# Performance work log

Measured on AMD Instinct MI355X. Metric: run time of the kernel, lower is better.

## Reference

```python
import jax, jax.numpy as jnp
import numpy as np
from jax import lax

IMG_SIZE = 512        # efficientdet-d0 input resolution
TOP_K = 256           # fixed candidate count for jit-compatible NMS
THRESHOLD = 0.01      # score threshold (init kwarg)
IOU_THRESHOLD = 0.5   # NMS IoU threshold (init kwarg)


def make_anchors():
    """Standard EfficientDet-d0 anchors: P3-P7, 3 scales x 3 ratios, xyxy."""
    strides = [8, 16, 32, 64, 128]
    scales = [2.0 ** 0, 2.0 ** (1.0 / 3.0), 2.0 ** (2.0 / 3.0)]
    ratios = [0.5, 1.0, 2.0]
    base = 4.0
    out = []
    for s in strides:
        fs = IMG_SIZE // s
        xs = (np.arange(fs, dtype=np.float32) + 0.5) * s
        cy, cx = np.meshgrid(xs, xs, indexing='ij')
        for r in ratios:
            for sc in scales:
                w = base * s * sc * np.sqrt(1.0 / r)
                h = base * s * sc * np.sqrt(r)
                a = np.stack([cx - w / 2, cy - h / 2, cx + w / 2, cy + h / 2], -1)
                out.append(a.reshape(-1, 4))
    return np.concatenate(out, 0).astype(np.float32)  # [49104, 4]


def decode_boxes(anchors, regs):
    """RetinaNet-style delta decode. anchors [A,4] xyxy, regs [B,A,4]."""
    aw = anchors[:, 2] - anchors[:, 0]
    ah = anchors[:, 3] - anchors[:, 1]
    acx = anchors[:, 0] + 0.5 * aw
    acy = anchors[:, 1] + 0.5 * ah
    dx, dy, dw, dh = regs[..., 0], regs[..., 1], regs[..., 2], regs[..., 3]
    cx = acx + dx * aw
    cy = acy + dy * ah
    w = aw * jnp.exp(jnp.clip(dw, -4.0, 4.0))
    h = ah * jnp.exp(jnp.clip(dh, -4.0, 4.0))
    boxes = jnp.stack([cx - 0.5 * w, cy - 0.5 * h, cx + 0.5 * w, cy + 0.5 * h], -1)
    return jnp.clip(boxes, 0.0, float(IMG_SIZE))  # [B,A,4]


def pairwise_iou(boxes):
    """boxes [K,4] xyxy -> iou [K,K]."""
    area = jnp.maximum(boxes[:, 2] - boxes[:, 0], 0) * jnp.maximum(boxes[:, 3] - boxes[:, 1], 0)
    lt = jnp.maximum(boxes[:, None, :2], boxes[None, :, :2])
    rb = jnp.minimum(boxes[:, None, 2:], boxes[None, :, 2:])
    wh = jnp.maximum(rb - lt, 0.0)
    inter = wh[..., 0] * wh[..., 1]
    union = area[:, None] + area[None, :] - inter
    return inter / jnp.maximum(union, 1e-8)


def nms_keep(boxes, scores):
    """Sequential NMS over score-sorted candidates. boxes [K,4], scores [K]."""
    K = boxes.shape[0]
    iou = pairwise_iou(boxes)  # [K,K]
    ar = jnp.arange(K)
    keep0 = scores > 0.0

    def body(i, keep):
        suppressed = jnp.any(keep & (iou[:, i] > IOU_THRESHOLD) & (ar < i))
        return keep.at[i].set(keep[i] & ~suppressed)

    return lax.fori_loop(0, K, body, keep0)


def setup_inputs() -> dict:
    key = jax.random.key(0)
    k1, k2 = jax.random.split(key)
    B, A, C = 8, 49104, 80
    cls_logits = jax.random.normal(k1, (B, A, C), dtype=jnp.float32) - 2.0
    box_regs = 0.2 * jax.random.normal(k2, (B, A, 4), dtype=jnp.float32)
    anchors = jnp.asarray(make_anchors())
    return {"cls_logits": cls_logits, "box_regs": box_regs, "anchors": anchors}


def reference(cls_logits, box_regs, anchors):
    probs = jax.nn.sigmoid(cls_logits)            # [B,A,C]
    scores = probs.max(-1)                        # [B,A]
    labels = probs.argmax(-1)                     # [B,A]
    boxes = decode_boxes(anchors, box_regs)       # [B,A,4]
    scores = jnp.where(scores > THRESHOLD, scores, 0.0)
    top_s, idx = lax.top_k(scores, TOP_K)         # [B,K]
    top_b = jnp.take_along_axis(boxes, idx[..., None], axis=1)   # [B,K,4]
    top_l = jnp.take_along_axis(labels, idx, axis=1)             # [B,K]
    keep = jax.vmap(nms_keep)(top_b, top_s)                      # [B,K] bool
    keep_f = keep.astype(top_b.dtype)
    dets = jnp.concatenate([top_b * keep_f[..., None], (top_s * keep_f)[..., None]], -1)  # [B,K,5]
    return dets, top_l, keep
```

## Files before the change

### kernel.cpp

```cpp
#include <hip/hip_runtime.h>
#include <stdint.h>
#include <math.h>

#define IMGF   512.0f
#define A_N    49104
#define B_N    8
#define C_N    80
#define K_N    256
#define IOU_T  0.5f
#define NBIN   4096
#define CAP    2048

__device__ __forceinline__ int bin_of(uint32_t key) {
    float s = __uint_as_float(key);
    int b = (int)(s * 4096.0f);
    return b > 4095 ? 4095 : b;
}

__global__ __launch_bounds__(256) void score_kernel(
    const float* __restrict__ logits,
    uint32_t* __restrict__ keys)
{
    const int tid  = threadIdx.x;
    const int lane = tid & 63;
    const int grp  = lane >> 2, j = lane & 3;
    const int g = blockIdx.x * 64 + (tid >> 6) * 16 + grp;

    const float4* p = (const float4*)(logits + (size_t)g * C_N);
    float4 v0 = p[j], v1 = p[j + 4], v2 = p[j + 8], v3 = p[j + 12], v4 = p[j + 16];
    float m = fmaxf(fmaxf(fmaxf(v0.x, v0.y), fmaxf(v0.z, v0.w)),
                    fmaxf(fmaxf(v1.x, v1.y), fmaxf(v1.z, v1.w)));
    m = fmaxf(m, fmaxf(fmaxf(v2.x, v2.y), fmaxf(v2.z, v2.w)));
    m = fmaxf(m, fmaxf(fmaxf(v3.x, v3.y), fmaxf(v3.z, v3.w)));
    m = fmaxf(m, fmaxf(fmaxf(v4.x, v4.y), fmaxf(v4.z, v4.w)));
    m = fmaxf(m, __shfl_xor(m, 1, 64));
    m = fmaxf(m, __shfl_xor(m, 2, 64));
    if (j == 0) {
        float s = 1.0f / (1.0f + expf(-m));
        if (!(s > 0.01f)) s = 0.0f;
        keys[g] = __float_as_uint(s);
    }
}

__global__ __launch_bounds__(1024) void select_nms_kernel(
    const uint32_t* __restrict__ keys,
    const float* __restrict__ logits,
    const float* __restrict__ regs,
    const float* __restrict__ anchors,
    float* __restrict__ out)
{
    const int b   = blockIdx.x;
    const int tid = threadIdx.x;
    const int lane = tid & 63, wv = tid >> 6;

    __shared__ uint32_t hist[NBIN];
    __shared__ int wtots[16];
    __shared__ int sh_T, sh_nc;
    __shared__ unsigned long long cand[CAP];
    __shared__ unsigned long long sorted[K_N];
    __shared__ float4 sbox[K_N];
    __shared__ float  sscore[K_N];
    __shared__ int    slab[K_N];
    __shared__ unsigned long long supr[K_N][4];
    __shared__ unsigned long long keepw[4];

    const uint32_t* kb = keys + (size_t)b * A_N;
    const uint4* kb4 = (const uint4*)kb;
    const int N4 = A_N / 4;

    for (int i = tid; i < NBIN; i += 1024) hist[i] = 0;
    if (tid == 0) sh_nc = 0;
    __syncthreads();
    for (int i = tid; i < N4; i += 1024) {
        uint4 v = kb4[i];
        atomicAdd(&hist[bin_of(v.x)], 1u);
        atomicAdd(&hist[bin_of(v.y)], 1u);
        atomicAdd(&hist[bin_of(v.z)], 1u);
        atomicAdd(&hist[bin_of(v.w)], 1u);
    }
    __syncthreads();

    const int lo = tid * 4;
    int seg = (int)hist[lo] + (int)hist[lo + 1]
            + (int)hist[lo + 2] + (int)hist[lo + 3];
    int s1 = seg;
#pragma unroll
    for (int off = 1; off < 64; off <<= 1) {
        int v = __shfl_down(s1, off, 64);
        if (lane + off < 64) s1 += v;
    }
    if (lane == 0) wtots[wv] = s1;
    __syncthreads();
    int wsuf = 0;
    for (int w = wv + 1; w < 16; ++w) wsuf += wtots[w];
    int above = wsuf + (s1 - seg);
    if (above < K_N && above + seg >= K_N) {
        int cum = above;
        for (int bin = lo + 3; bin >= lo; --bin) {
            int c = (int)hist[bin];
            if (cum + c >= K_N) { sh_T = bin; break; }
            cum += c;
        }
    }
    __syncthreads();
    const int T = sh_T;

    for (int i = tid; i < N4; i += 1024) {
        uint4 v = kb4[i];
        uint32_t ks[4] = { v.x, v.y, v.z, v.w };
#pragma unroll
        for (int q = 0; q < 4; ++q) {
            if (bin_of(ks[q]) >= T) {
                int p = atomicAdd(&sh_nc, 1);
                if (p < CAP)
                    cand[p] = ((unsigned long long)ks[q] << 32)
                            | (unsigned long long)(0xFFFFFFFFu - (uint32_t)(4 * i + q));
            }
        }
    }
    if (tid < K_N) sorted[tid] = 0ull;
    __syncthreads();
    int nc = sh_nc; if (nc > CAP) nc = CAP;

    for (int i = tid; i < nc; i += 1024) {
        unsigned long long me = cand[i];
        int r = 0;
        for (int jq = 0; jq < nc; ++jq) r += (cand[jq] > me);
        if (r < K_N) sorted[r] = me;
    }
    __syncthreads();

    if (tid < K_N) {
#pragma clang fp contract(off)
        unsigned long long cv = sorted[tid];
        uint32_t key = (uint32_t)(cv >> 32);
        uint32_t ai  = 0xFFFFFFFFu - (uint32_t)cv;
        if (ai >= (uint32_t)A_N) ai = 0;
        int a = (int)ai;
        float s = __uint_as_float(key);
        sscore[tid] = s;

        {
            const float4* lp = (const float4*)(logits + ((size_t)b * A_N + a) * C_N);
            float best = -INFINITY; int cls = 0;
#pragma unroll
            for (int k = 0; k < 20; ++k) {
                float4 w = lp[k];
                if (w.x > best) { best = w.x; cls = 4 * k + 0; }
                if (w.y > best) { best = w.y; cls = 4 * k + 1; }
                if (w.z > best) { best = w.z; cls = 4 * k + 2; }
                if (w.w > best) { best = w.w; cls = 4 * k + 3; }
            }
            slab[tid] = cls;
        }

        float ax0 = anchors[4 * a + 0], ay0 = anchors[4 * a + 1];
        float ax1 = anchors[4 * a + 2], ay1 = anchors[4 * a + 3];
        float aw = ax1 - ax0, ah = ay1 - ay0;
        float acx = ax0 + 0.5f * aw, acy = ay0 + 0.5f * ah;
        const float* r = regs + ((size_t)b * A_N + a) * 4;
        float dx = r[0], dy = r[1], dw = r[2], dh = r[3];
        float cx = acx + dx * aw;
        float cy = acy + dy * ah;
        dw = fminf(fmaxf(dw, -4.0f), 4.0f);
        dh = fminf(fmaxf(dh, -4.0f), 4.0f);
        float w = aw * expf(dw);
        float h = ah * expf(dh);
        float x0 = cx - 0.5f * w, y0 = cy - 0.5f * h;
        float x1 = cx + 0.5f * w, y1 = cy + 0.5f * h;
        x0 = fminf(fmaxf(x0, 0.0f), IMGF);
        y0 = fminf(fmaxf(y0, 0.0f), IMGF);
        x1 = fminf(fmaxf(x1, 0.0f), IMGF);
        y1 = fminf(fmaxf(y1, 0.0f), IMGF);
        sbox[tid] = make_float4(x0, y0, x1, y1);
    }
    __syncthreads();

    {
#pragma clang fp contract(off)
        const int row = tid & 255, gq = tid >> 8;
        float4 bi = sbox[row];
        float areai = fmaxf(bi.z - bi.x, 0.0f) * fmaxf(bi.w - bi.y, 0.0f);
        unsigned long long m = 0;
        const int jlo = gq * 64, jhi = jlo + 64;
        int start = row + 1 > jlo ? row + 1 : jlo;
        for (int jx = start; jx < jhi; ++jx) {
            float4 bj = sbox[jx];
            float areaj = fmaxf(bj.z - bj.x, 0.0f) * fmaxf(bj.w - bj.y, 0.0f);
            float lx = fmaxf(bi.x, bj.x), ly = fmaxf(bi.y, bj.y);
            float rx = fminf(bi.z, bj.z), ry = fminf(bi.w, bj.w);
            float iw = fmaxf(rx - lx, 0.0f), ih = fmaxf(ry - ly, 0.0f);
            float inter = iw * ih;
            float uni = areai + areaj - inter;
            float iou = inter / fmaxf(uni, 1e-8f);
            if (iou > IOU_T) m |= 1ull << (jx & 63);
        }
        supr[row][gq] = m;
    }
    if (tid < K_N) {
        unsigned long long ball = __ballot(sscore[tid] > 0.0f);
        if ((tid & 63) == 0) keepw[tid >> 6] = ball;
    }
    __syncthreads();

    if (tid == 0) {
        unsigned long long k0 = keepw[0], k1 = keepw[1], k2 = keepw[2], k3 = keepw[3];
#define NMS_CHUNK(c, kc)                                                     \
        for (int l = 0; l < 64; ++l) {                                       \
            const int i = (c) * 64 + l;                                      \
            unsigned long long w0 = supr[i][0], w1 = supr[i][1];             \
            unsigned long long w2 = supr[i][2], w3 = supr[i][3];             \
            if ((kc >> l) & 1ull) {                                          \
                k0 &= ~w0; k1 &= ~w1; k2 &= ~w2; k3 &= ~w3;                  \
            }                                                                \
        }
        NMS_CHUNK(0, k0)
        NMS_CHUNK(1, k1)
        NMS_CHUNK(2, k2)
        NMS_CHUNK(3, k3)
#undef NMS_CHUNK
        keepw[0] = k0; keepw[1] = k1; keepw[2] = k2; keepw[3] = k3;
    }
    __syncthreads();

    if (tid < K_N) {
        float keepf = ((keepw[tid >> 6] >> (tid & 63)) & 1ull) ? 1.0f : 0.0f;
        float4 bx = sbox[tid];
        float s = sscore[tid];
        float* det = out + ((size_t)b * K_N + tid) * 5;
        det[0] = bx.x * keepf;
        det[1] = bx.y * keepf;
        det[2] = bx.z * keepf;
        det[3] = bx.w * keepf;
        det[4] = s * keepf;
        out[(size_t)B_N * K_N * 5 + (size_t)b * K_N + tid] = (float)slab[tid];
        out[(size_t)B_N * K_N * 5 + (size_t)B_N * K_N + (size_t)b * K_N + tid] = keepf;
    }
}

extern "C" void kernel_launch(void* const* d_in, const int* in_sizes, int n_in,
                              void* d_out, int out_size, void* d_ws, size_t ws_size,
                              hipStream_t stream)
{
    const float* logits  = (const float*)d_in[0];
    const float* regs    = (const float*)d_in[1];
    const float* anchors = (const float*)d_in[2];
    float* out = (float*)d_out;

    uint32_t* keys = (uint32_t*)d_ws;

    const int total = B_N * A_N;
    score_kernel<<<total / 64, 256, 0, stream>>>(logits, keys);
    select_nms_kernel<<<B_N, 1024, 0, stream>>>(keys, logits, regs, anchors, out);
}
```

Measured before the change: 239.5 us.

## Build per-batch score histogram in score kernel with global atomics

Moves the 4096-bin score histogram out of the single-block-per-batch select kernel into the wide score kernel, using global atomics into a workspace buffer that is zeroed with a memset each launch. The select kernel then reads its four bins per thread directly, which removes a full pass over the keys and the shared-memory atomics from the 8-block serial stage. It also vectorises the anchor and regression loads to float4. The cost is an extra memset launch plus contention on global atomics, since most scores fall into a few low bins.

```diff
diff --git a/kernel.cpp b/kernel.cpp
--- a/kernel.cpp
+++ b/kernel.cpp
@@ -19,7 +19,8 @@
 
 __global__ __launch_bounds__(256) void score_kernel(
     const float* __restrict__ logits,
-    uint32_t* __restrict__ keys)
+    uint32_t* __restrict__ keys,
+    uint32_t* __restrict__ ghist)
 {
     const int tid  = threadIdx.x;
     const int lane = tid & 63;
@@ -39,11 +40,16 @@
         float s = 1.0f / (1.0f + expf(-m));
         if (!(s > 0.01f)) s = 0.0f;
         keys[g] = __float_as_uint(s);
+        int b = g / A_N;
+        int bin = (int)(s * 4096.0f);
+        if (bin > 4095) bin = 4095;
+        atomicAdd(&ghist[(b << 12) + bin], 1u);
     }
 }
 
 __global__ __launch_bounds__(1024) void select_nms_kernel(
     const uint32_t* __restrict__ keys,
+    const uint32_t* __restrict__ ghist,
     const float* __restrict__ logits,
     const float* __restrict__ regs,
     const float* __restrict__ anchors,
@@ -53,7 +59,6 @@
     const int tid = threadIdx.x;
     const int lane = tid & 63, wv = tid >> 6;
 
-    __shared__ uint32_t hist[NBIN];
     __shared__ int wtots[16];
     __shared__ int sh_T, sh_nc;
     __shared__ unsigned long long cand[CAP];
@@ -68,21 +73,12 @@
     const uint4* kb4 = (const uint4*)kb;
     const int N4 = A_N / 4;
 
-    for (int i = tid; i < NBIN; i += 1024) hist[i] = 0;
     if (tid == 0) sh_nc = 0;
-    __syncthreads();
-    for (int i = tid; i < N4; i += 1024) {
-        uint4 v = kb4[i];
-        atomicAdd(&hist[bin_of(v.x)], 1u);
-        atomicAdd(&hist[bin_of(v.y)], 1u);
-        atomicAdd(&hist[bin_of(v.z)], 1u);
-        atomicAdd(&hist[bin_of(v.w)], 1u);
-    }
-    __syncthreads();
-
+
+    const uint4 hv = ((const uint4*)(ghist + ((size_t)b << 12)))[tid];
+    const int c0 = (int)hv.x, c1 = (int)hv.y, c2 = (int)hv.z, c3 = (int)hv.w;
     const int lo = tid * 4;
-    int seg = (int)hist[lo] + (int)hist[lo + 1]
-            + (int)hist[lo + 2] + (int)hist[lo + 3];
+    int seg = c0 + c1 + c2 + c3;
     int s1 = seg;
 #pragma unroll
     for (int off = 1; off < 64; off <<= 1) {
@@ -95,12 +91,10 @@
     for (int w = wv + 1; w < 16; ++w) wsuf += wtots[w];
     int above = wsuf + (s1 - seg);
     if (above < K_N && above + seg >= K_N) {
-        int cum = above;
-        for (int bin = lo + 3; bin >= lo; --bin) {
-            int c = (int)hist[bin];
-            if (cum + c >= K_N) { sh_T = bin; break; }
-            cum += c;
-        }
+        if      (above + c3 >= K_N)           sh_T = lo + 3;
+        else if (above + c3 + c2 >= K_N)      sh_T = lo + 2;
+        else if (above + c3 + c2 + c1 >= K_N) sh_T = lo + 1;
+        else                                  sh_T = lo;
     }
     __syncthreads();
     const int T = sh_T;
@@ -154,12 +148,12 @@
             slab[tid] = cls;
         }
 
-        float ax0 = anchors[4 * a + 0], ay0 = anchors[4 * a + 1];
-        float ax1 = anchors[4 * a + 2], ay1 = anchors[4 * a + 3];
+        float4 av = ((const float4*)anchors)[a];
+        float ax0 = av.x, ay0 = av.y, ax1 = av.z, ay1 = av.w;
         float aw = ax1 - ax0, ah = ay1 - ay0;
         float acx = ax0 + 0.5f * aw, acy = ay0 + 0.5f * ah;
-        const float* r = regs + ((size_t)b * A_N + a) * 4;
-        float dx = r[0], dy = r[1], dw = r[2], dh = r[3];
+        float4 rv = ((const float4*)regs)[(size_t)b * A_N + a];
+        float dx = rv.x, dy = rv.y, dw = rv.z, dh = rv.w;
         float cx = acx + dx * aw;
         float cy = acy + dy * ah;
         dw = fminf(fmaxf(dw, -4.0f), 4.0f);
@@ -247,9 +241,12 @@
     const float* anchors = (const float*)d_in[2];
     float* out = (float*)d_out;
 
-    uint32_t* keys = (uint32_t*)d_ws;
+    uint32_t* keys  = (uint32_t*)d_ws;
+    uint32_t* ghist = keys + (size_t)B_N * A_N;
+
+    hipMemsetAsync(ghist, 0, (size_t)B_N * NBIN * sizeof(uint32_t), stream);
 
     const int total = B_N * A_N;
-    score_kernel<<<total / 64, 256, 0, stream>>>(logits, keys);
-    select_nms_kernel<<<B_N, 1024, 0, stream>>>(keys, logits, regs, anchors, out);
-}
+    score_kernel<<<total / 64, 256, 0, stream>>>(logits, keys, ghist);
+    select_nms_kernel<<<B_N, 1024, 0, stream>>>(keys, ghist, logits, regs, anchors, out);
+}
```

Result: slower. 258.1 us (+7.8%).
